# Optimization experiments

Hardware: AMD Instinct MI355X
Metric: run time of the kernel (lower is better)

## Reference

```python
import jax, jax.numpy as jnp
import numpy as np

PI = 3.141592653589793
TAU = 2.0      # tau for both rpe_lif (spikingjelly default 2.0) and act_conv (params['tau'])
V_TH = 1.0     # spikingjelly LIFNode default v_threshold
EPS = 1e-5     # LayerNorm / BatchNorm eps


@jax.custom_vjp
def atan_spike(x):
    # Heaviside forward, ATan surrogate backward (spikingjelly surrogate.ATan, alpha=2)
    return (x >= 0.0).astype(x.dtype)

def _atan_fwd(x):
    return atan_spike(x), x

def _atan_bwd(x, g):
    # (alpha/2) / (1 + ((pi/2)*alpha*x)^2) with alpha=2 -> 1/(1+(pi*x)^2)
    return (g / (1.0 + (PI * x) ** 2),)

atan_spike.defvjp(_atan_fwd, _atan_bwd)


def lif(x_seq, tau=TAU):
    """Multi-step LIF: decay_input=True, v_reset=0, hard reset, detach_reset.
    x_seq: [T, ...]; returns spikes [T, ...]."""
    def step(v, x):
        v = v + (x - v) / tau                      # neuronal charge
        s = atan_spike(v - V_TH)                   # fire
        v = v * (1.0 - jax.lax.stop_gradient(s))   # detached hard reset to 0
        return v, s
    _, spikes = jax.lax.scan(step, jnp.zeros_like(x_seq[0]), x_seq)
    return spikes


def setup_inputs() -> dict:
    key = jax.random.key(0)
    ks = jax.random.split(key, 8)
    B, L, D, T = 256, 50, 128, 4
    n_items, n_h, n_v = 100001, 8, 4
    emb = jax.random.normal(ks[0], (n_items, D), jnp.float32) * 0.5
    emb = emb.at[0].set(0.0)  # padding_idx=0
    return {
        "item_seq": jax.random.randint(ks[1], (B, L), 0, n_items, jnp.int32),
        "emb_table": emb,
        "ln_gamma": jnp.ones((D,), jnp.float32),
        "ln_beta": jnp.zeros((D,), jnp.float32),
        "conv_v_w": jax.random.normal(ks[2], (n_v, L), jnp.float32) * float(1.0 / np.sqrt(L)),
        # per-length kernels stored padded: kernel for length k=i+1 is conv_h_w[i, :, :k, :]
        "conv_h_w": jax.random.normal(ks[3], (L, n_h, L, D), jnp.float32) * 0.02,
        "bn_gamma": jnp.ones((L, n_h), jnp.float32),
        "bn_beta": jnp.zeros((L, n_h), jnp.float32),
        "fc_h_w": jax.random.normal(ks[4], (D, n_h * L), jnp.float32) * 0.05,
        "fc_h_b": jnp.zeros((D,), jnp.float32),
        "fc_v_w": jax.random.normal(ks[5], (D, n_v * D), jnp.float32) * 0.04,
        "fc_v_b": jnp.zeros((D,), jnp.float32),
        "T": 4,
    }


def reference(item_seq, emb_table, ln_gamma, ln_beta, conv_v_w, conv_h_w,
              bn_gamma, bn_beta, fc_h_w, fc_h_b, fc_v_w, fc_v_b, T):
    B, L = item_seq.shape
    D = emb_table.shape[1]
    n_h = conv_h_w.shape[1]
    n_v = conv_v_w.shape[0]

    # embedding + LayerNorm
    emb = emb_table[item_seq]                                   # [B,L,D]
    mu = emb.mean(-1, keepdims=True)
    var = emb.var(-1, keepdims=True)
    x = (emb - mu) / jnp.sqrt(var + EPS) * ln_gamma + ln_beta   # [B,L,D]

    # repeat over T and spike (rpe_lif)
    s = lif(jnp.broadcast_to(x, (T, B, L, D)))                  # binary spikes [T,B,L,D]

    # vertical conv: kernel (L,1), no bias -> collapses seq axis
    out_v = jnp.einsum('tbld,cl->tbcd', s, conv_v_w).reshape(T, B, n_v * D)

    # horizontal multi-scale convs + BN(train stats) + LIF + global max pool
    s2 = s.reshape(T * B, 1, L, D)
    pools = []
    for i in range(L):
        k = i + 1
        w = conv_h_w[i, :, :k, :][:, None]                      # [n_h,1,k,D]
        y = jax.lax.conv_general_dilated(
            s2, w, (1, 1), 'VALID',
            dimension_numbers=('NCHW', 'OIHW', 'NCHW'))[:, :, :, 0]  # [TB,n_h,L-k+1]
        m = y.mean(axis=(0, 2))                                  # BN over (T*B, spatial)
        v = y.var(axis=(0, 2))
        y = (y - m[:, None]) * (bn_gamma[i][:, None] / jnp.sqrt(v[:, None] + EPS)) + bn_beta[i][:, None]
        y = lif(y.reshape(T, B, n_h, L - k + 1))                 # [T,B,n_h,L-k+1]
        pools.append(y.max(axis=-1))                             # [T,B,n_h]
    out_h = jnp.concatenate(pools, axis=-1)                      # [T,B,n_h*L]

    out_h = (out_h @ fc_h_w.T + fc_h_b).mean(0)                  # [B,D]
    out_v = out_v.mean(0) @ fc_v_w.T + fc_v_b                    # [B,D]
    return out_h + out_v
```

## Files before the change

kernel.cpp:

```cpp
#include <hip/hip_runtime.h>

#define B_ 256
#define L_ 50
#define D_ 128
#define T_ 4
#define NH 8
#define NV 4
#define TB_ (T_*B_)
#define EPSF 1e-5f

typedef _Float16 h8 __attribute__((ext_vector_type(8)));
typedef float f4 __attribute__((ext_vector_type(4)));

__device__ __forceinline__ float waveSum(float v) {
    #pragma unroll
    for (int o = 32; o > 0; o >>= 1) v += __shfl_down(v, o, 64);
    return v;
}

__device__ __forceinline__ size_t yoff(int i) {
    return (size_t)8192 * (size_t)(50 * i - (i * (i - 1)) / 2);
}

__global__ __launch_bounds__(256) void k0_wsplit(
        const float* __restrict__ w, _Float16* __restrict__ whl) {
    int dk = blockIdx.x, i = blockIdx.y;
    int t = threadIdx.x;
    int c = t >> 4, gd = t & 15;
    int h = c & 7;
    bool live = (i < 50) && (dk <= i);
    const float* src = w + (((size_t)i * NH + h) * L_ + dk) * D_ + gd * 8;
    h8 o;
    #pragma unroll
    for (int e = 0; e < 8; ++e) {
        float wv = live ? src[e] : 0.f;
        _Float16 hi = (_Float16)wv;
        o[e] = (c < 8) ? hi : (_Float16)((wv - (float)hi) * 1024.f);
    }
    *(h8*)(whl + (((size_t)i * 50 + dk) * 16 + c) * 128 + ((gd ^ c) & 15) * 8) = o;
}

__global__ __launch_bounds__(128) void k1_embed_ln_lif(
        const int* __restrict__ item, const float* __restrict__ tab,
        const float* __restrict__ g, const float* __restrict__ be,
        _Float16* __restrict__ s16, float* __restrict__ smean) {
    int bid = blockIdx.x;
    int b = bid / L_, l = bid % L_;
    int d = threadIdx.x;
    int wid = d >> 6, lane = d & 63;
    __shared__ float red[2];
    int it = item[b * L_ + l];
    float e = tab[(size_t)it * D_ + d];
    float sm_ = waveSum(e);
    if (lane == 0) red[wid] = sm_;
    __syncthreads();
    float mu = (red[0] + red[1]) * (1.f / 128.f);
    __syncthreads();
    float df = e - mu;
    float s2 = waveSum(df * df);
    if (lane == 0) red[wid] = s2;
    __syncthreads();
    float var = (red[0] + red[1]) * (1.f / 128.f);
    float x = df / sqrtf(var + EPSF) * g[d] + be[d];
    float v = 0.f, acc = 0.f;
    int pos = (((d >> 3) ^ l) & 15) * 8 + (d & 7);
    #pragma unroll
    for (int t = 0; t < T_; ++t) {
        v += (x - v) * 0.5f;
        float sp = (v >= 1.f) ? 1.f : 0.f;
        v *= (1.f - sp);
        s16[((size_t)(t * B_ + b) * L_ + l) * D_ + pos] = (_Float16)sp;
        acc += sp;
    }
    smean[((size_t)b * L_ + l) * D_ + d] = acc * 0.25f;
}

template<int MTG>
__global__ __launch_bounds__(512, 2) void k2w(
        const _Float16* __restrict__ s16, const _Float16* __restrict__ whl,
        float* __restrict__ y, int gbase, int joff) {
    extern __shared__ __align__(16) char lds[];
    const int tbo = blockIdx.x;
    const int i0 = (gbase + blockIdx.y) * 4;
    const int kmax = (i0 + 4 <= 50) ? (i0 + 4) : 50;
    const int tid = threadIdx.x;
    const int wave = tid >> 6, lane = tid & 63;
    const int tq = wave >> 2;
    const int dc = wave & 3;
    const int c_ = lane & 15, g = lane >> 4;

    {
        const float4* src = (const float4*)(s16 + (size_t)tbo * 8 * (L_ * D_));
        float4* dst = (float4*)lds;
        for (int idx = tid; idx < 6400; idx += 512) dst[idx] = src[idx];
    }

    const int boffc = c_ * 256 + ((((dc << 2) + g) ^ c_) & 15) * 16;
    const char* gB = (const char*)whl + (size_t)i0 * 204800 + boffc;

    h8 bf0 = *(const h8*)(gB);
    h8 bf1 = *(const h8*)(gB + 204800);
    h8 bf2 = *(const h8*)(gB + 409600);
    h8 bf3 = *(const h8*)(gB + 614400);
    __syncthreads();

    f4 acc[4][4][MTG];
    #pragma unroll
    for (int sc = 0; sc < 4; ++sc)
        #pragma unroll
        for (int tt = 0; tt < 4; ++tt)
            #pragma unroll
            for (int jt = 0; jt < MTG; ++jt) { f4 z = {0.f, 0.f, 0.f, 0.f}; acc[sc][tt][jt] = z; }

    for (int dk = 0; dk < kmax; ++dk) {
        const bool more = (dk + 1 < kmax);
        h8 bn0, bn1, bn2, bn3;
        if (more) {
            const char* p = gB + (size_t)(dk + 1) * 4096;
            bn0 = *(const h8*)(p);
            bn1 = *(const h8*)(p + 204800);
            bn2 = *(const h8*)(p + 409600);
            bn3 = *(const h8*)(p + 614400);
        }
        #pragma unroll
        for (int tt = 0; tt < 4; ++tt) {
            const int tbL = tq * 4 + tt;
            #pragma unroll
            for (int jt = 0; jt < MTG; ++jt) {
                int l = (joff + jt) * 16 + c_ + dk; if (l > 49) l = 49;
                h8 a = *(const h8*)(lds + tbL * 12800 + l * 256 +
                                    ((((dc << 2) + g) ^ l) & 15) * 16);
                acc[0][tt][jt] = __builtin_amdgcn_mfma_f32_16x16x32_f16(a, bf0, acc[0][tt][jt], 0, 0, 0);
                acc[1][tt][jt] = __builtin_amdgcn_mfma_f32_16x16x32_f16(a, bf1, acc[1][tt][jt], 0, 0, 0);
                acc[2][tt][jt] = __builtin_amdgcn_mfma_f32_16x16x32_f16(a, bf2, acc[2][tt][jt], 0, 0, 0);
                acc[3][tt][jt] = __builtin_amdgcn_mfma_f32_16x16x32_f16(a, bf3, acc[3][tt][jt], 0, 0, 0);
            }
        }
        bf0 = bn0; bf1 = bn1; bf2 = bn2; bf3 = bn3;
    }

    f4* mbuf = (f4*)lds;
    #pragma unroll
    for (int jt = 0; jt < MTG; ++jt) {
        __syncthreads();
        if (dc != 0) {
            f4* wp = mbuf + (size_t)(((dc - 1) * 2 + tq) * 16) * 64 + lane;
            #pragma unroll
            for (int sc = 0; sc < 4; ++sc)
                #pragma unroll
                for (int tt = 0; tt < 4; ++tt)
                    wp[(sc * 4 + tt) * 64] = acc[sc][tt][jt];
        }
        __syncthreads();
        if (dc == 0) {
            #pragma unroll
            for (int dd = 0; dd < 3; ++dd) {
                const f4* rp = mbuf + (size_t)((dd * 2 + tq) * 16) * 64 + lane;
                #pragma unroll
                for (int sc = 0; sc < 4; ++sc)
                    #pragma unroll
                    for (int tt = 0; tt < 4; ++tt)
                        acc[sc][tt][jt] += rp[(sc * 4 + tt) * 64];
            }
        }
    }

    if (dc == 0) {
        const bool hiLane = (c_ < 8);
        const int h = c_ & 7;
        #pragma unroll
        for (int sc = 0; sc < 4; ++sc) {
            const int i = i0 + sc;
            const int J = 50 - i;
            if (J <= 0) continue;
            #pragma unroll
            for (int tt = 0; tt < 4; ++tt) {
                const int tb = tbo * 8 + tq * 4 + tt;
                size_t yb = yoff(i) + ((size_t)tb * NH + h) * J;
                #pragma unroll
                for (int jt = 0; jt < MTG; ++jt) {
                    #pragma unroll
                    for (int r = 0; r < 4; ++r) {
                        float lo = __shfl_xor(acc[sc][tt][jt][r], 8, 64);
                        int j = (joff + jt) * 16 + g * 4 + r;
                        if (hiLane && j < J) y[yb + j] = acc[sc][tt][jt][r] + lo * (1.f / 1024.f);
                    }
                }
            }
        }
    }
}

__global__ __launch_bounds__(256) void k3_partial(
        const float* __restrict__ y, float* __restrict__ psum) {
    int ih = blockIdx.x, ck = blockIdx.y;
    int i = ih >> 3, h = ih & 7;
    int J = 50 - i;
    size_t yb = yoff(i);
    int tid = threadIdx.x;
    int grp = tid >> 5, sub = tid & 31;
    float sm = 0.f, ss = 0.f;
    for (int tb = ck * 128 + grp; tb < (ck + 1) * 128; tb += 8) {
        const float* row = y + yb + ((size_t)tb * NH + h) * J;
        for (int j = sub; j < J; j += 32) { float v = row[j]; sm += v; ss += v * v; }
    }
    __shared__ float r1[4], r2[4];
    float a = waveSum(sm), b = waveSum(ss);
    int wid = tid >> 6, lane = tid & 63;
    if (lane == 0) { r1[wid] = a; r2[wid] = b; }
    __syncthreads();
    if (tid == 0) {
        psum[((size_t)ih * 8 + ck) * 2]     = r1[0] + r1[1] + r1[2] + r1[3];
        psum[((size_t)ih * 8 + ck) * 2 + 1] = r2[0] + r2[1] + r2[2] + r2[3];
    }
}

__global__ __launch_bounds__(256) void k3_final(
        const float* __restrict__ psum, const float* __restrict__ bng,
        float* __restrict__ statm, float* __restrict__ stats_) {
    int ih = blockIdx.x * 256 + threadIdx.x;
    if (ih >= 400) return;
    float S = 0.f, Q = 0.f;
    for (int ck = 0; ck < 8; ++ck) {
        S += psum[((size_t)ih * 8 + ck) * 2];
        Q += psum[((size_t)ih * 8 + ck) * 2 + 1];
    }
    int i = ih >> 3;
    float cnt = 1024.f * (float)(50 - i);
    float m = S / cnt;
    float var = Q / cnt - m * m; if (var < 0.f) var = 0.f;
    statm[ih] = m;
    stats_[ih] = bng[ih] / sqrtf(var + EPSF);
}

__global__ __launch_bounds__(512) void k4_bn_lif_pool(
        const float* __restrict__ y, const float* __restrict__ statm,
        const float* __restrict__ stats_, const float* __restrict__ bnb,
        float* __restrict__ ps) {
    int b = blockIdx.x, i = blockIdx.y, J = L_ - i;
    int h = threadIdx.x >> 6, lane = threadIdx.x & 63;
    int ih = i * NH + h;
    float m = statm[ih], sc = stats_[ih], bb = bnb[ih];
    size_t yb = yoff(i);
    bool valid = lane < J;
    float v = 0.f; int cnt = 0;
    #pragma unroll
    for (int t = 0; t < T_; ++t) {
        int tb = t * B_ + b;
        float yn;
        if (valid) {
            float raw = y[yb + ((size_t)tb * NH + h) * J + lane];
            yn = (raw - m) * sc + bb;
        } else yn = -1e30f;
        v += (yn - v) * 0.5f;
        bool sp = (v >= 1.f);
        if (sp) v = 0.f;
        if (__any(sp)) cnt++;
    }
    if (lane == 0) ps[(size_t)b * 400 + ih] = (float)cnt;
}

__global__ __launch_bounds__(128) void k5_final(
        const float* __restrict__ smean, const float* __restrict__ ps,
        const float* __restrict__ convv, const float* __restrict__ fchw,
        const float* __restrict__ fchb, const float* __restrict__ fcvw,
        const float* __restrict__ fcvb, float* __restrict__ out) {
    __shared__ float sm_l[L_ * D_];
    __shared__ float vm[NV * D_];
    __shared__ float ps_l[400];
    int b = blockIdx.x, tid = threadIdx.x;
    for (int idx = tid; idx < L_ * D_; idx += 128) sm_l[idx] = smean[(size_t)b * (L_ * D_) + idx];
    for (int idx = tid; idx < 400; idx += 128) ps_l[idx] = ps[(size_t)b * 400 + idx];
    __syncthreads();
    int d = tid;
    #pragma unroll
    for (int c = 0; c < NV; ++c) {
        float a = 0.f;
        for (int l = 0; l < L_; ++l) a += convv[c * L_ + l] * sm_l[l * D_ + d];
        vm[c * D_ + d] = a;
    }
    __syncthreads();
    float acc = fchb[d] + fcvb[d];
    float ah = 0.f;
    for (int ih = 0; ih < 400; ++ih) ah += ps_l[ih] * fchw[d * 400 + ih];
    acc += ah * 0.25f;
    float av = 0.f;
    for (int cd = 0; cd < NV * D_; ++cd) av += vm[cd] * fcvw[d * (NV * D_) + cd];
    acc += av;
    out[(size_t)b * D_ + d] = acc;
}

extern "C" void kernel_launch(void* const* d_in, const int* in_sizes, int n_in,
                              void* d_out, int out_size, void* d_ws, size_t ws_size,
                              hipStream_t stream) {
    const int*   item  = (const int*)d_in[0];
    const float* tab   = (const float*)d_in[1];
    const float* lng   = (const float*)d_in[2];
    const float* lnb   = (const float*)d_in[3];
    const float* convv = (const float*)d_in[4];
    const float* convh = (const float*)d_in[5];
    const float* bng   = (const float*)d_in[6];
    const float* bnb   = (const float*)d_in[7];
    const float* fchw  = (const float*)d_in[8];
    const float* fchb  = (const float*)d_in[9];
    const float* fcvw  = (const float*)d_in[10];
    const float* fcvb  = (const float*)d_in[11];
    float* out = (float*)d_out;

    char* ws = (char*)d_ws;
    _Float16* s16  = (_Float16*)(ws);
    float* smean   = (float*)(ws + 13107200LL);
    float* y       = (float*)(ws + 19660800LL);
    _Float16* whl  = (_Float16*)(ws + 61440000LL);
    float* statm   = (float*)(ws + 72089600LL);
    float* stats_  = (float*)(ws + 72091200LL);
    float* ps      = (float*)(ws + 72092800LL);
    float* psum    = (float*)(ws + 72502400LL);

    hipFuncSetAttribute(reinterpret_cast<const void*>(&k2w<1>),
        hipFuncAttributeMaxDynamicSharedMemorySize, 102400);
    hipFuncSetAttribute(reinterpret_cast<const void*>(&k2w<2>),
        hipFuncAttributeMaxDynamicSharedMemorySize, 102400);

    k0_wsplit<<<dim3(50, 52), 256, 0, stream>>>(convh, whl);
    k1_embed_ln_lif<<<B_ * L_, 128, 0, stream>>>(item, tab, lng, lnb, s16, smean);
    k2w<2><<<dim3(128, 1), 512, 102400, stream>>>(s16, whl, y, 0, 0);
    k2w<2><<<dim3(128, 1), 512, 102400, stream>>>(s16, whl, y, 0, 2);
    k2w<2><<<dim3(128, 4), 512, 102400, stream>>>(s16, whl, y, 1, 0);
    k2w<1><<<dim3(128, 4), 512, 102400, stream>>>(s16, whl, y, 1, 2);
    k2w<2><<<dim3(128, 4), 512, 102400, stream>>>(s16, whl, y, 5, 0);
    k2w<1><<<dim3(128, 4), 512, 102400, stream>>>(s16, whl, y, 9, 0);
    k3_partial<<<dim3(400, 8), 256, 0, stream>>>(y, psum);
    k3_final<<<dim3(2, 1), 256, 0, stream>>>(psum, bng, statm, stats_);
    k4_bn_lif_pool<<<dim3(B_, L_), 512, 0, stream>>>(y, statm, stats_, bnb, ps);
    k5_final<<<B_, 128, 0, stream>>>(smean, ps, convv, fchw, fchb, fcvw, fcvb, out);
}
```

Measured before the change: 320.4 us.

## Halve conv tile per block and merge six conv launches into two

The horizontal-conv MFMA kernel now handles 4 (T*B) rows per block instead of 8. This halves LDS use to 51200 bytes and the accumulator register count, and launch bounds are raised to allow 4 blocks per CU. The six separate group launches are folded into two launches that decode the group and column offset from blockIdx.y, removing launch overhead and tail gaps. In exchange, each weight fragment loaded from global memory is reused across half as many rows, so weight traffic per block rises relative to compute.

```diff
diff --git a/kernel.cpp b/kernel.cpp
--- a/kernel.cpp
+++ b/kernel.cpp
@@ -76,12 +76,20 @@
 }
 
 template<int MTG>
-__global__ __launch_bounds__(512, 2) void k2w(
+__global__ __launch_bounds__(512, 4) void k2x(
         const _Float16* __restrict__ s16, const _Float16* __restrict__ whl,
-        float* __restrict__ y, int gbase, int joff) {
+        float* __restrict__ y, int mode) {
     extern __shared__ __align__(16) char lds[];
-    const int tbo = blockIdx.x;
-    const int i0 = (gbase + blockIdx.y) * 4;
+    const int tbq = blockIdx.x;
+    int grp, joff;
+    if (mode == 0) {
+        if (blockIdx.y < 2) { grp = 0; joff = 2 * blockIdx.y; }
+        else { grp = blockIdx.y - 1; joff = 0; }
+    } else {
+        if (blockIdx.y < 4) { grp = blockIdx.y + 1; joff = 2; }
+        else { grp = blockIdx.y + 5; joff = 0; }
+    }
+    const int i0 = grp * 4;
     const int kmax = (i0 + 4 <= 50) ? (i0 + 4) : 50;
     const int tid = threadIdx.x;
     const int wave = tid >> 6, lane = tid & 63;
@@ -90,9 +98,9 @@
     const int c_ = lane & 15, g = lane >> 4;
 
     {
-        const float4* src = (const float4*)(s16 + (size_t)tbo * 8 * (L_ * D_));
+        const float4* src = (const float4*)(s16 + (size_t)tbq * 4 * (L_ * D_));
         float4* dst = (float4*)lds;
-        for (int idx = tid; idx < 6400; idx += 512) dst[idx] = src[idx];
+        for (int idx = tid; idx < 3200; idx += 512) dst[idx] = src[idx];
     }
 
     const int boffc = c_ * 256 + ((((dc << 2) + g) ^ c_) & 15) * 16;
@@ -104,11 +112,11 @@
     h8 bf3 = *(const h8*)(gB + 614400);
     __syncthreads();
 
-    f4 acc[4][4][MTG];
+    f4 acc[4][2][MTG];
     #pragma unroll
     for (int sc = 0; sc < 4; ++sc)
         #pragma unroll
-        for (int tt = 0; tt < 4; ++tt)
+        for (int tt = 0; tt < 2; ++tt)
             #pragma unroll
             for (int jt = 0; jt < MTG; ++jt) { f4 z = {0.f, 0.f, 0.f, 0.f}; acc[sc][tt][jt] = z; }
 
@@ -123,8 +131,8 @@
             bn3 = *(const h8*)(p + 614400);
         }
         #pragma unroll
-        for (int tt = 0; tt < 4; ++tt) {
-            const int tbL = tq * 4 + tt;
+        for (int tt = 0; tt < 2; ++tt) {
+            const int tbL = tq * 2 + tt;
             #pragma unroll
             for (int jt = 0; jt < MTG; ++jt) {
                 int l = (joff + jt) * 16 + c_ + dk; if (l > 49) l = 49;
@@ -144,23 +152,23 @@
     for (int jt = 0; jt < MTG; ++jt) {
         __syncthreads();
         if (dc != 0) {
-            f4* wp = mbuf + (size_t)(((dc - 1) * 2 + tq) * 16) * 64 + lane;
+            f4* wp = mbuf + (size_t)(((dc - 1) * 2 + tq) * 8) * 64 + lane;
             #pragma unroll
             for (int sc = 0; sc < 4; ++sc)
                 #pragma unroll
-                for (int tt = 0; tt < 4; ++tt)
-                    wp[(sc * 4 + tt) * 64] = acc[sc][tt][jt];
+                for (int tt = 0; tt < 2; ++tt)
+                    wp[(sc * 2 + tt) * 64] = acc[sc][tt][jt];
         }
         __syncthreads();
         if (dc == 0) {
             #pragma unroll
             for (int dd = 0; dd < 3; ++dd) {
-                const f4* rp = mbuf + (size_t)((dd * 2 + tq) * 16) * 64 + lane;
+                const f4* rp = mbuf + (size_t)((dd * 2 + tq) * 8) * 64 + lane;
                 #pragma unroll
                 for (int sc = 0; sc < 4; ++sc)
                     #pragma unroll
-                    for (int tt = 0; tt < 4; ++tt)
-                        acc[sc][tt][jt] += rp[(sc * 4 + tt) * 64];
+                    for (int tt = 0; tt < 2; ++tt)
+                        acc[sc][tt][jt] += rp[(sc * 2 + tt) * 64];
             }
         }
     }
@@ -174,8 +182,8 @@
             const int J = 50 - i;
             if (J <= 0) continue;
             #pragma unroll
-            for (int tt = 0; tt < 4; ++tt) {
-                const int tb = tbo * 8 + tq * 4 + tt;
+            for (int tt = 0; tt < 2; ++tt) {
+                const int tb = tbq * 4 + tq * 2 + tt;
                 size_t yb = yoff(i) + ((size_t)tb * NH + h) * J;
                 #pragma unroll
                 for (int jt = 0; jt < MTG; ++jt) {
@@ -317,19 +325,10 @@
     float* ps      = (float*)(ws + 72092800LL);
     float* psum    = (float*)(ws + 72502400LL);
 
-    hipFuncSetAttribute(reinterpret_cast<const void*>(&k2w<1>),
-        hipFuncAttributeMaxDynamicSharedMemorySize, 102400);
-    hipFuncSetAttribute(reinterpret_cast<const void*>(&k2w<2>),
-        hipFuncAttributeMaxDynamicSharedMemorySize, 102400);
-
     k0_wsplit<<<dim3(50, 52), 256, 0, stream>>>(convh, whl);
     k1_embed_ln_lif<<<B_ * L_, 128, 0, stream>>>(item, tab, lng, lnb, s16, smean);
-    k2w<2><<<dim3(128, 1), 512, 102400, stream>>>(s16, whl, y, 0, 0);
-    k2w<2><<<dim3(128, 1), 512, 102400, stream>>>(s16, whl, y, 0, 2);
-    k2w<2><<<dim3(128, 4), 512, 102400, stream>>>(s16, whl, y, 1, 0);
-    k2w<1><<<dim3(128, 4), 512, 102400, stream>>>(s16, whl, y, 1, 2);
-    k2w<2><<<dim3(128, 4), 512, 102400, stream>>>(s16, whl, y, 5, 0);
-    k2w<1><<<dim3(128, 4), 512, 102400, stream>>>(s16, whl, y, 9, 0);
+    k2x<2><<<dim3(256, 10), 512, 51200, stream>>>(s16, whl, y, 0);
+    k2x<1><<<dim3(256, 8), 512, 51200, stream>>>(s16, whl, y, 1);
     k3_partial<<<dim3(400, 8), 256, 0, stream>>>(y, psum);
     k3_final<<<dim3(2, 1), 256, 0, stream>>>(psum, bng, statm, stats_);
     k4_bn_lif_pool<<<dim3(B_, L_), 512, 0, stream>>>(y, statm, stats_, bnb, ps);
```

Measured after the change: 311.6 us. 1.03x faster.

## Merge conv GEMM launches into one table-driven grid with double-buffered operands

Applied to the files above, without the earlier changes.

Replaces the six templated k2w launches with a single k2z launch. Its grid y-dimension indexes a lookup table of (i0, j-window) pairs, ordered with the heaviest work items first. Each block now handles one 16-wide output column window. The inner loop is unrolled by two, with A (from LDS) and B (from global) fragments double-buffered and sched_barriers placed to overlap loads with MFMAs. This aims to cut launch and tail overhead and hide load latency, at the cost of reloading the LDS tile for every column window. The odd-kmax tail reads one past-the-end B row, which is harmless because it stays within the workspace.

```diff
diff --git a/kernel.cpp b/kernel.cpp
--- a/kernel.cpp
+++ b/kernel.cpp
@@ -75,19 +75,28 @@
     smean[((size_t)b * L_ + l) * D_ + d] = acc * 0.25f;
 }
 
-template<int MTG>
-__global__ __launch_bounds__(512, 2) void k2w(
+
+__device__ const int JZ_i0[28] = {
+    48, 44, 40, 36, 32, 32, 28, 28, 24, 24, 20, 20,
+    16, 16, 16, 12, 12, 12,  8,  8,  8,  4,  4,  4,  0,  0,  0,  0};
+__device__ const int JZ_jw[28] = {
+     0,  0,  0,  0,  0,  1,  0,  1,  0,  1,  0,  1,
+     0,  1,  2,  0,  1,  2,  0,  1,  2,  0,  1,  2,  0,  1,  2,  3};
+
+__global__ __launch_bounds__(512, 2) void k2z(
         const _Float16* __restrict__ s16, const _Float16* __restrict__ whl,
-        float* __restrict__ y, int gbase, int joff) {
+        float* __restrict__ y) {
     extern __shared__ __align__(16) char lds[];
     const int tbo = blockIdx.x;
-    const int i0 = (gbase + blockIdx.y) * 4;
+    const int i0 = JZ_i0[blockIdx.y];
+    const int jw = JZ_jw[blockIdx.y];
     const int kmax = (i0 + 4 <= 50) ? (i0 + 4) : 50;
     const int tid = threadIdx.x;
     const int wave = tid >> 6, lane = tid & 63;
     const int tq = wave >> 2;
     const int dc = wave & 3;
     const int c_ = lane & 15, g = lane >> 4;
+    const int dcg = (dc << 2) + g;
 
     {
         const float4* src = (const float4*)(s16 + (size_t)tbo * 8 * (L_ * D_));
@@ -95,77 +104,97 @@
         for (int idx = tid; idx < 6400; idx += 512) dst[idx] = src[idx];
     }
 
-    const int boffc = c_ * 256 + ((((dc << 2) + g) ^ c_) & 15) * 16;
+    const int boffc = c_ * 256 + ((dcg ^ c_) & 15) * 16;
     const char* gB = (const char*)whl + (size_t)i0 * 204800 + boffc;
-
-    h8 bf0 = *(const h8*)(gB);
-    h8 bf1 = *(const h8*)(gB + 204800);
-    h8 bf2 = *(const h8*)(gB + 409600);
-    h8 bf3 = *(const h8*)(gB + 614400);
-    __syncthreads();
-
-    f4 acc[4][4][MTG];
+    const char* ldsA = lds + tq * 4 * 12800;
+
+    h8 aC[4], aN[4], bC[4], bN[4];
+    bC[0] = *(const h8*)(gB);
+    bC[1] = *(const h8*)(gB + 204800);
+    bC[2] = *(const h8*)(gB + 409600);
+    bC[3] = *(const h8*)(gB + 614400);
+    __syncthreads();
+    {
+        int l = jw * 16 + c_; if (l > 49) l = 49;
+        const int ao = l * 256 + ((dcg ^ l) & 15) * 16;
+        aC[0] = *(const h8*)(ldsA + ao);
+        aC[1] = *(const h8*)(ldsA + 12800 + ao);
+        aC[2] = *(const h8*)(ldsA + 25600 + ao);
+        aC[3] = *(const h8*)(ldsA + 38400 + ao);
+    }
+
+    f4 acc[4][4];
     #pragma unroll
     for (int sc = 0; sc < 4; ++sc)
         #pragma unroll
-        for (int tt = 0; tt < 4; ++tt)
+        for (int tt = 0; tt < 4; ++tt) { f4 z = {0.f, 0.f, 0.f, 0.f}; acc[sc][tt] = z; }
+
+    for (int dk = 0; dk < kmax; dk += 2) {
+        {
+            const char* p = gB + (size_t)(dk + 1) * 4096;
+            bN[0] = *(const h8*)(p);
+            bN[1] = *(const h8*)(p + 204800);
+            bN[2] = *(const h8*)(p + 409600);
+            bN[3] = *(const h8*)(p + 614400);
+            int l = jw * 16 + c_ + dk + 1; if (l > 49) l = 49;
+            const int ao = l * 256 + ((dcg ^ l) & 15) * 16;
+            aN[0] = *(const h8*)(ldsA + ao);
+            aN[1] = *(const h8*)(ldsA + 12800 + ao);
+            aN[2] = *(const h8*)(ldsA + 25600 + ao);
+            aN[3] = *(const h8*)(ldsA + 38400 + ao);
+        }
+        __builtin_amdgcn_sched_barrier(0);
+        #pragma unroll
+        for (int tt = 0; tt < 4; ++tt) {
+            acc[0][tt] = __builtin_amdgcn_mfma_f32_16x16x32_f16(aC[tt], bC[0], acc[0][tt], 0, 0, 0);
+            acc[1][tt] = __builtin_amdgcn_mfma_f32_16x16x32_f16(aC[tt], bC[1], acc[1][tt], 0, 0, 0);
+            acc[2][tt] = __builtin_amdgcn_mfma_f32_16x16x32_f16(aC[tt], bC[2], acc[2][tt], 0, 0, 0);
+            acc[3][tt] = __builtin_amdgcn_mfma_f32_16x16x32_f16(aC[tt], bC[3], acc[3][tt], 0, 0, 0);
+        }
+        if (dk + 2 < kmax) {
+            const char* p = gB + (size_t)(dk + 2) * 4096;
+            bC[0] = *(const h8*)(p);
+            bC[1] = *(const h8*)(p + 204800);
+            bC[2] = *(const h8*)(p + 409600);
+            bC[3] = *(const h8*)(p + 614400);
+            int l = jw * 16 + c_ + dk + 2; if (l > 49) l = 49;
+            const int ao = l * 256 + ((dcg ^ l) & 15) * 16;
+            aC[0] = *(const h8*)(ldsA + ao);
+            aC[1] = *(const h8*)(ldsA + 12800 + ao);
+            aC[2] = *(const h8*)(ldsA + 25600 + ao);
+            aC[3] = *(const h8*)(ldsA + 38400 + ao);
+        }
+        __builtin_amdgcn_sched_barrier(0);
+        #pragma unroll
+        for (int tt = 0; tt < 4; ++tt) {
+            acc[0][tt] = __builtin_amdgcn_mfma_f32_16x16x32_f16(aN[tt], bN[0], acc[0][tt], 0, 0, 0);
+            acc[1][tt] = __builtin_amdgcn_mfma_f32_16x16x32_f16(aN[tt], bN[1], acc[1][tt], 0, 0, 0);
+            acc[2][tt] = __builtin_amdgcn_mfma_f32_16x16x32_f16(aN[tt], bN[2], acc[2][tt], 0, 0, 0);
+            acc[3][tt] = __builtin_amdgcn_mfma_f32_16x16x32_f16(aN[tt], bN[3], acc[3][tt], 0, 0, 0);
+        }
+    }
+
+    __syncthreads();
+    f4* mbuf = (f4*)lds;
+    if (dc != 0) {
+        f4* wp = mbuf + (size_t)(((dc - 1) * 2 + tq) * 16) * 64 + lane;
+        #pragma unroll
+        for (int sc = 0; sc < 4; ++sc)
             #pragma unroll
-            for (int jt = 0; jt < MTG; ++jt) { f4 z = {0.f, 0.f, 0.f, 0.f}; acc[sc][tt][jt] = z; }
-
-    for (int dk = 0; dk < kmax; ++dk) {
-        const bool more = (dk + 1 < kmax);
-        h8 bn0, bn1, bn2, bn3;
-        if (more) {
-            const char* p = gB + (size_t)(dk + 1) * 4096;
-            bn0 = *(const h8*)(p);
-            bn1 = *(const h8*)(p + 204800);
-            bn2 = *(const h8*)(p + 409600);
-            bn3 = *(const h8*)(p + 614400);
-        }
-        #pragma unroll
-        for (int tt = 0; tt < 4; ++tt) {
-            const int tbL = tq * 4 + tt;
-            #pragma unroll
-            for (int jt = 0; jt < MTG; ++jt) {
-                int l = (joff + jt) * 16 + c_ + dk; if (l > 49) l = 49;
-                h8 a = *(const h8*)(lds + tbL * 12800 + l * 256 +
-                                    ((((dc << 2) + g) ^ l) & 15) * 16);
-                acc[0][tt][jt] = __builtin_amdgcn_mfma_f32_16x16x32_f16(a, bf0, acc[0][tt][jt], 0, 0, 0);
-                acc[1][tt][jt] = __builtin_amdgcn_mfma_f32_16x16x32_f16(a, bf1, acc[1][tt][jt], 0, 0, 0);
-                acc[2][tt][jt] = __builtin_amdgcn_mfma_f32_16x16x32_f16(a, bf2, acc[2][tt][jt], 0, 0, 0);
-                acc[3][tt][jt] = __builtin_amdgcn_mfma_f32_16x16x32_f16(a, bf3, acc[3][tt][jt], 0, 0, 0);
-            }
-        }
-        bf0 = bn0; bf1 = bn1; bf2 = bn2; bf3 = bn3;
-    }
-
-    f4* mbuf = (f4*)lds;
-    #pragma unroll
-    for (int jt = 0; jt < MTG; ++jt) {
-        __syncthreads();
-        if (dc != 0) {
-            f4* wp = mbuf + (size_t)(((dc - 1) * 2 + tq) * 16) * 64 + lane;
+            for (int tt = 0; tt < 4; ++tt)
+                wp[(sc * 4 + tt) * 64] = acc[sc][tt];
+    }
+    __syncthreads();
+    if (dc == 0) {
+        #pragma unroll
+        for (int dd = 0; dd < 3; ++dd) {
+            const f4* rp = mbuf + (size_t)((dd * 2 + tq) * 16) * 64 + lane;
             #pragma unroll
             for (int sc = 0; sc < 4; ++sc)
                 #pragma unroll
                 for (int tt = 0; tt < 4; ++tt)
-                    wp[(sc * 4 + tt) * 64] = acc[sc][tt][jt];
-        }
-        __syncthreads();
-        if (dc == 0) {
-            #pragma unroll
-            for (int dd = 0; dd < 3; ++dd) {
-                const f4* rp = mbuf + (size_t)((dd * 2 + tq) * 16) * 64 + lane;
-                #pragma unroll
-                for (int sc = 0; sc < 4; ++sc)
-                    #pragma unroll
-                    for (int tt = 0; tt < 4; ++tt)
-                        acc[sc][tt][jt] += rp[(sc * 4 + tt) * 64];
-            }
-        }
-    }
-
-    if (dc == 0) {
+                    acc[sc][tt] += rp[(sc * 4 + tt) * 64];
+        }
         const bool hiLane = (c_ < 8);
         const int h = c_ & 7;
         #pragma unroll
@@ -178,13 +207,10 @@
                 const int tb = tbo * 8 + tq * 4 + tt;
                 size_t yb = yoff(i) + ((size_t)tb * NH + h) * J;
                 #pragma unroll
-                for (int jt = 0; jt < MTG; ++jt) {
-                    #pragma unroll
-                    for (int r = 0; r < 4; ++r) {
-                        float lo = __shfl_xor(acc[sc][tt][jt][r], 8, 64);
-                        int j = (joff + jt) * 16 + g * 4 + r;
-                        if (hiLane && j < J) y[yb + j] = acc[sc][tt][jt][r] + lo * (1.f / 1024.f);
-                    }
+                for (int r = 0; r < 4; ++r) {
+                    float lo = __shfl_xor(acc[sc][tt][r], 8, 64);
+                    int j = jw * 16 + g * 4 + r;
+                    if (hiLane && j < J) y[yb + j] = acc[sc][tt][r] + lo * (1.f / 1024.f);
                 }
             }
         }
@@ -317,19 +343,12 @@
     float* ps      = (float*)(ws + 72092800LL);
     float* psum    = (float*)(ws + 72502400LL);
 
-    hipFuncSetAttribute(reinterpret_cast<const void*>(&k2w<1>),
-        hipFuncAttributeMaxDynamicSharedMemorySize, 102400);
-    hipFuncSetAttribute(reinterpret_cast<const void*>(&k2w<2>),
+    hipFuncSetAttribute(reinterpret_cast<const void*>(&k2z),
         hipFuncAttributeMaxDynamicSharedMemorySize, 102400);
 
     k0_wsplit<<<dim3(50, 52), 256, 0, stream>>>(convh, whl);
     k1_embed_ln_lif<<<B_ * L_, 128, 0, stream>>>(item, tab, lng, lnb, s16, smean);
-    k2w<2><<<dim3(128, 1), 512, 102400, stream>>>(s16, whl, y, 0, 0);
-    k2w<2><<<dim3(128, 1), 512, 102400, stream>>>(s16, whl, y, 0, 2);
-    k2w<2><<<dim3(128, 4), 512, 102400, stream>>>(s16, whl, y, 1, 0);
-    k2w<1><<<dim3(128, 4), 512, 102400, stream>>>(s16, whl, y, 1, 2);
-    k2w<2><<<dim3(128, 4), 512, 102400, stream>>>(s16, whl, y, 5, 0);
-    k2w<1><<<dim3(128, 4), 512, 102400, stream>>>(s16, whl, y, 9, 0);
+    k2z<<<dim3(128, 28), 512, 102400, stream>>>(s16, whl, y);
     k3_partial<<<dim3(400, 8), 256, 0, stream>>>(y, psum);
     k3_final<<<dim3(2, 1), 256, 0, stream>>>(psum, bng, statm, stats_);
     k4_bn_lif_pool<<<dim3(B_, L_), 512, 0, stream>>>(y, statm, stats_, bnb, ps);
```

Result: faster. 302.9 us (-5.4%).
